# Kernel optimization log

Hardware: AMD Instinct MI355X
Metric: run time of the kernel (lower is better)

## Reference

```python
import jax, jax.numpy as jnp
import numpy as np

C = 256
HEADS = 8
HD = C // HEADS
EPS = 1e-5


def _layernorm(x, g, b):
    mu = jnp.mean(x, axis=-1, keepdims=True)
    var = jnp.var(x, axis=-1, keepdims=True)
    return (x - mu) * jax.lax.rsqrt(var + EPS) * g + b


def setup_inputs() -> dict:
    key = jax.random.key(0)
    ks = jax.random.split(key, 16)
    s = 0.02
    return {
        "x": jax.random.normal(ks[0], (1, C, 64, 64), jnp.float32),
        "bn_gamma": 1.0 + s * jax.random.normal(ks[1], (C,), jnp.float32),
        "bn_beta": s * jax.random.normal(ks[2], (C,), jnp.float32),
        "bn_mean": s * jax.random.normal(ks[3], (C,), jnp.float32),
        "bn_var": jnp.ones((C,), jnp.float32),
        "w_in": s * jax.random.normal(ks[4], (C, C), jnp.float32),
        "b_in": jnp.zeros((C,), jnp.float32),
        "ln1_g": jnp.ones((C,), jnp.float32),
        "ln1_b": jnp.zeros((C,), jnp.float32),
        "w_qkv": s * jax.random.normal(ks[5], (3 * C, C), jnp.float32),
        "b_qkv": jnp.zeros((3 * C,), jnp.float32),
        "w_ap": s * jax.random.normal(ks[6], (C, C), jnp.float32),
        "b_ap": jnp.zeros((C,), jnp.float32),
        "ln2_g": jnp.ones((C,), jnp.float32),
        "ln2_b": jnp.zeros((C,), jnp.float32),
        "w_ff1": s * jax.random.normal(ks[7], (4 * C, C), jnp.float32),
        "b_ff1": jnp.zeros((4 * C,), jnp.float32),
        "w_ff2": s * jax.random.normal(ks[8], (C, 4 * C), jnp.float32),
        "b_ff2": jnp.zeros((C,), jnp.float32),
        "w_out": s * jax.random.normal(ks[9], (C, C), jnp.float32),
        "b_out": jnp.zeros((C,), jnp.float32),
    }


def reference(x, bn_gamma, bn_beta, bn_mean, bn_var, w_in, b_in,
              ln1_g, ln1_b, w_qkv, b_qkv, w_ap, b_ap,
              ln2_g, ln2_b, w_ff1, b_ff1, w_ff2, b_ff2, w_out, b_out):
    b, c, h, w = x.shape
    t = h * w
    x_in = x
    # BatchNorm2d (eval mode: running stats)
    xn = (x - bn_mean[None, :, None, None]) * jax.lax.rsqrt(bn_var + EPS)[None, :, None, None]
    xn = xn * bn_gamma[None, :, None, None] + bn_beta[None, :, None, None]
    # proj_in 1x1 conv -> tokens [b, t, c]
    tok = xn.reshape(b, c, t).transpose(0, 2, 1)
    tok = tok @ w_in.T + b_in
    # transformer block (depth=1)
    y = _layernorm(tok, ln1_g, ln1_b)  # norm1
    qkv = y @ w_qkv.T + b_qkv  # [b, t, 3c], channel split (3, H, hd)
    qkv = qkv.reshape(b, t, 3, HEADS, HD)
    q = qkv[:, :, 0].transpose(0, 2, 1, 3)  # [b, H, t, hd]
    k = qkv[:, :, 1].transpose(0, 2, 1, 3)
    v = qkv[:, :, 2].transpose(0, 2, 1, 3)
    scale = HD ** (-0.5)
    attn = jax.nn.softmax(jnp.einsum('bhqd,bhkd->bhqk', q, k) * scale, axis=-1)
    o = jnp.einsum('bhqk,bhkd->bhqd', attn, v)  # [b, H, t, hd]
    o = o.transpose(0, 2, 1, 3).reshape(b, t, c)  # channels ordered (H, hd)
    o = o @ w_ap.T + b_ap  # attn proj 1x1
    attn_out = o + y  # VanillaAttention residual adds its (normed) input
    tok = tok + attn_out
    # FFN
    z = _layernorm(tok, ln2_g, ln2_b)
    z = jax.nn.gelu(z @ w_ff1.T + b_ff1, approximate=False)
    tok = tok + (z @ w_ff2.T + b_ff2)
    # back to image, proj_out 1x1, outer residual
    x4 = tok.transpose(0, 2, 1).reshape(b, c, h, w)
    out = jnp.einsum('oc,bchw->bohw', w_out, x4) + b_out[None, :, None, None]
    return out + x_in
```

## Files before the change

### kernel.cpp

```cpp
#include <hip/hip_runtime.h>
#include <math.h>

#define T_TOK 4096
#define C_DIM 256
#define EPSF  1e-5f
#define SC_QL (0.17677669529663687f * 1.4426950408889634f)

typedef short  bf16x8  __attribute__((ext_vector_type(8)));
typedef float  f32x4   __attribute__((ext_vector_type(4)));
typedef ushort ushort8 __attribute__((ext_vector_type(8)));

__device__ __forceinline__ short f2bf(float f) {
    unsigned u = __builtin_bit_cast(unsigned, f);
    unsigned r = (u + 0x7FFFu + ((u >> 16) & 1u)) >> 16;
    return (short)r;
}
__device__ __forceinline__ float bf2f(ushort u) {
    return __builtin_bit_cast(float, ((unsigned)u) << 16);
}
__device__ __forceinline__ unsigned pk_bf16(float a, float b) {
    const unsigned ua = __builtin_bit_cast(unsigned, a) + 0x8000u;
    const unsigned ub = __builtin_bit_cast(unsigned, b) + 0x8000u;
    return __builtin_amdgcn_perm(ub, ua, 0x07060302u);
}
#define MFMA16(a, b, c) __builtin_amdgcn_mfma_f32_16x16x32_bf16(a, b, c, 0, 0, 0)

__global__ __launch_bounds__(256) void prep_kernel(
    const float* __restrict__ w_in, const float* __restrict__ w_qkv,
    const float* __restrict__ w_ap, const float* __restrict__ w_ff1,
    const float* __restrict__ w_ff2, const float* __restrict__ w_out,
    const float* __restrict__ b_qkv, const float* __restrict__ b_ff1,
    const float* __restrict__ ln1_g, const float* __restrict__ ln1_b,
    const float* __restrict__ ln2_g, const float* __restrict__ ln2_b,
    ushort* __restrict__ wbuf, float* __restrict__ u_all, float* __restrict__ d_all,
    const float* __restrict__ x, const float* __restrict__ gamma,
    const float* __restrict__ beta, const float* __restrict__ mean,
    const float* __restrict__ var, ushort* __restrict__ tin)
{
    __shared__ float tile[32][33];
    if (blockIdx.x < 896) {
        const int gid = blockIdx.x * 256 + threadIdx.x;
        const int e0 = gid * 4;
        const float* src; int off;
        float4 sc = {1.f, 1.f, 1.f, 1.f};
        if (e0 < 65536)       { src = w_in;  off = e0; }
        else if (e0 < 262144) {
            src = w_qkv; off = e0 - 65536;
            sc = *(const float4*)(ln1_g + (off & 255));
            if (off < 65536) { sc.x *= SC_QL; sc.y *= SC_QL; sc.z *= SC_QL; sc.w *= SC_QL; }
        }
        else if (e0 < 327680) { src = w_ap;  off = e0 - 262144; }
        else if (e0 < 589824) {
            src = w_ff1; off = e0 - 327680;
            sc = *(const float4*)(ln2_g + (off & 255));
        }
        else if (e0 < 851968) { src = w_ff2; off = e0 - 589824; }
        else                  { src = w_out; off = e0 - 851968; }
        const float4 v = *(const float4*)(src + off);
        ushort4 o;
        o.x = (ushort)f2bf(v.x * sc.x); o.y = (ushort)f2bf(v.y * sc.y);
        o.z = (ushort)f2bf(v.z * sc.z); o.w = (ushort)f2bf(v.w * sc.w);
        *(ushort4*)(wbuf + e0) = o;
    } else if (blockIdx.x < 1920) {
        const int bidx = blockIdx.x - 896;
        const int t0 = (bidx & 127) * 32, c0 = (bidx >> 7) * 32;
        const int tx = threadIdx.x & 31, ty = threadIdx.x >> 5;
#pragma unroll
        for (int i = 0; i < 32; i += 8) {
            const int c = c0 + ty + i;
            const float a = rsqrtf(var[c] + EPSF) * gamma[c];
            const float d = beta[c] - mean[c] * a;
            tile[ty + i][tx] = x[c * T_TOK + t0 + tx] * a + d;
        }
        __syncthreads();
#pragma unroll
        for (int i = 0; i < 32; i += 8) {
            const int t = t0 + ty + i;
            tin[t * C_DIM + c0 + tx] = (ushort)f2bf(tile[tx][ty + i]);
        }
    } else {
        const int row = (blockIdx.x - 1920) * 4 + (threadIdx.x >> 6);
        const int lane = threadIdx.x & 63;
        const float* W; const float* gv; const float* bv; float bias; float qs = 1.f;
        if (row < 768) {
            W = w_qkv + (size_t)row * 256; gv = ln1_g; bv = ln1_b; bias = b_qkv[row];
            if (row < 256) qs = SC_QL;
        } else {
            const int r2 = row - 768;
            W = w_ff1 + (size_t)r2 * 256; gv = ln2_g; bv = ln2_b; bias = b_ff1[r2];
        }
        const float4 w4 = *(const float4*)(W + lane * 4);
        const float4 g4 = *(const float4*)(gv + lane * 4);
        const float4 b4 = *(const float4*)(bv + lane * 4);
        float su = w4.x * g4.x + w4.y * g4.y + w4.z * g4.z + w4.w * g4.w;
        float sd = w4.x * b4.x + w4.y * b4.y + w4.z * b4.z + w4.w * b4.w;
#pragma unroll
        for (int off = 32; off > 0; off >>= 1) {
            su += __shfl_xor(su, off);
            sd += __shfl_xor(sd, off);
        }
        if (lane == 0) {
            u_all[row] = qs * su;
            d_all[row] = qs * (sd + bias);
        }
    }
}

__global__ __launch_bounds__(256) void k_lnstats(
    const float* __restrict__ in, float* __restrict__ st)
{
    const int row = blockIdx.x * 4 + (threadIdx.x >> 6);
    const int lane = threadIdx.x & 63;
    const float4 v = *(const float4*)(in + (size_t)row * 256 + lane * 4);
    float s  = v.x + v.y + v.z + v.w;
    float s2 = v.x * v.x + v.y * v.y + v.z * v.z + v.w * v.w;
#pragma unroll
    for (int off = 32; off > 0; off >>= 1) {
        s  += __shfl_xor(s, off);
        s2 += __shfl_xor(s2, off);
    }
    if (lane == 0) {
        const float mu = s * (1.0f / 256.0f);
        const float var = s2 * (1.0f / 256.0f) - mu * mu;
        st[(size_t)row * 2 + 0] = mu;
        st[(size_t)row * 2 + 1] = rsqrtf(var + EPSF);
    }
}


__global__ __launch_bounds__(256) void k_proj_in(
    const ushort* __restrict__ tin, const ushort* __restrict__ wb,
    const float* __restrict__ bias, float* __restrict__ tok0,
    ushort* __restrict__ vbuf)
{
    __shared__ ushort At[16 * 264];
    const int chunk = blockIdx.x & 3, strip = blockIdx.x >> 2;
    const int tid = threadIdx.x, wv = tid >> 6, lane = tid & 63;
    const int c = lane & 15, g = lane >> 4;
    const int col = chunk * 64 + wv * 16 + c;
    const int t0 = strip * 16;

    bf16x8 w[8];
#pragma unroll
    for (int kc = 0; kc < 8; ++kc)
        w[kc] = *(const bf16x8*)(wb + (size_t)col * 256 + kc * 32 + g * 8);
    {
        const int r = tid >> 4, c0 = (tid & 15) * 16;
        *(ushort8*)&At[r * 264 + c0]     = *(const ushort8*)(tin + (size_t)(t0 + r) * 256 + c0);
        *(ushort8*)&At[r * 264 + c0 + 8] = *(const ushort8*)(tin + (size_t)(t0 + r) * 256 + c0 + 8);
    }
    __syncthreads();
    f32x4 acc = {};
#pragma unroll
    for (int kc = 0; kc < 8; ++kc)
        acc = MFMA16(*(const bf16x8*)&At[c * 264 + kc * 32 + g * 8], w[kc], acc);
    const float bb = bias[col];
#pragma unroll
    for (int rr = 0; rr < 4; ++rr) {
        const float v = acc[rr] + bb;
        const size_t idx = (size_t)(t0 + 4 * g + rr) * 256 + col;
        tok0[idx] = v;
        vbuf[idx] = (ushort)f2bf(v);
    }
}

__global__ __launch_bounds__(256) void k_qkv(
    const ushort* __restrict__ vbuf, const ushort* __restrict__ wb,
    const float* __restrict__ lnst, const float* __restrict__ u_all,
    const float* __restrict__ d_all, ushort* __restrict__ qkvb)
{
    __shared__ ushort At[2][16 * 264];
    const int chunk = blockIdx.x % 12, strip = blockIdx.x / 12;
    const int tid = threadIdx.x, wv = tid >> 6, lane = tid & 63;
    const int c = lane & 15, g = lane >> 4;
    const int col = chunk * 64 + wv * 16 + c;
    const int t0 = strip * 32;
    const int r = tid >> 4, c0 = (tid & 15) * 16;

    bf16x8 w[8];
#pragma unroll
    for (int kc = 0; kc < 8; ++kc)
        w[kc] = *(const bf16x8*)(wb + (size_t)col * 256 + kc * 32 + g * 8);
    ushort8 pre0 = *(const ushort8*)(vbuf + (size_t)(t0 + r) * 256 + c0);
    ushort8 pre1 = *(const ushort8*)(vbuf + (size_t)(t0 + r) * 256 + c0 + 8);

    const float u = u_all[col], d = d_all[col];
#pragma unroll
    for (int tile = 0; tile < 2; ++tile) {
        *(ushort8*)&At[tile][r * 264 + c0]     = pre0;
        *(ushort8*)&At[tile][r * 264 + c0 + 8] = pre1;
        __syncthreads();
        if (tile == 0) {
            pre0 = *(const ushort8*)(vbuf + (size_t)(t0 + 16 + r) * 256 + c0);
            pre1 = *(const ushort8*)(vbuf + (size_t)(t0 + 16 + r) * 256 + c0 + 8);
        }
        f32x4 acc = {};
#pragma unroll
        for (int kc = 0; kc < 8; ++kc)
            acc = MFMA16(*(const bf16x8*)&At[tile][c * 264 + kc * 32 + g * 8], w[kc], acc);
        const int tt = t0 + tile * 16;
#pragma unroll
        for (int rr = 0; rr < 4; ++rr) {
            const int row = tt + 4 * g + rr;
            const float mu = lnst[(size_t)row * 2 + 0];
            const float rs = lnst[(size_t)row * 2 + 1];
            qkvb[(size_t)row * 768 + col] = (ushort)f2bf(rs * (acc[rr] - mu * u) + d);
        }
    }
}

__global__ __launch_bounds__(256) void k_attnproj(
    const ushort* __restrict__ opart, const float* __restrict__ lpart,
    const ushort* __restrict__ wb, const float* __restrict__ bias,
    const float* __restrict__ tok0, const float* __restrict__ lnst,
    const float* __restrict__ ln1_g, const float* __restrict__ ln1_b,
    float* __restrict__ tok1, ushort* __restrict__ v2buf)
{
    __shared__ ushort At[16 * 264];
    const int chunk = blockIdx.x & 3, strip = blockIdx.x >> 2;
    const int tid = threadIdx.x, wv = tid >> 6, lane = tid & 63;
    const int c = lane & 15, g = lane >> 4;
    const int col = chunk * 64 + wv * 16 + c;
    const int t0 = strip * 16;

    bf16x8 w[8];
#pragma unroll
    for (int kc = 0; kc < 8; ++kc)
        w[kc] = *(const bf16x8*)(wb + (size_t)col * 256 + kc * 32 + g * 8);
    {
        const int r = tid >> 4, c0 = (tid & 15) * 16;
        const int hh = c0 >> 5;
        const float* lp = lpart + (size_t)(t0 + r) * 32;
        const float inv = 1.0f / (lp[hh] + lp[8 + hh] + lp[16 + hh] + lp[24 + hh]);
        const size_t base = (size_t)(t0 + r) * 256 + c0;
#pragma unroll
        for (int cc = 0; cc < 4; ++cc) {
            const ushort4 a0 = *(const ushort4*)(opart + base + cc * 4);
            const ushort4 a1 = *(const ushort4*)(opart + (1u << 20) + base + cc * 4);
            const ushort4 a2 = *(const ushort4*)(opart + (2u << 20) + base + cc * 4);
            const ushort4 a3 = *(const ushort4*)(opart + (3u << 20) + base + cc * 4);
            unsigned wpk[2];
            wpk[0] = pk_bf16((bf2f(a0.x) + bf2f(a1.x) + bf2f(a2.x) + bf2f(a3.x)) * inv,
                             (bf2f(a0.y) + bf2f(a1.y) + bf2f(a2.y) + bf2f(a3.y)) * inv);
            wpk[1] = pk_bf16((bf2f(a0.z) + bf2f(a1.z) + bf2f(a2.z) + bf2f(a3.z)) * inv,
                             (bf2f(a0.w) + bf2f(a1.w) + bf2f(a2.w) + bf2f(a3.w)) * inv);
            *(ushort4*)&At[r * 264 + c0 + cc * 4] = *(ushort4*)wpk;
        }
    }
    __syncthreads();
    f32x4 acc = {};
#pragma unroll
    for (int kc = 0; kc < 8; ++kc)
        acc = MFMA16(*(const bf16x8*)&At[c * 264 + kc * 32 + g * 8], w[kc], acc);
    const float bb = bias[col];
    const float g1 = ln1_g[col], b1 = ln1_b[col];
#pragma unroll
    for (int rr = 0; rr < 4; ++rr) {
        const int row = t0 + 4 * g + rr;
        const size_t idx = (size_t)row * 256 + col;
        const float t0v = tok0[idx];
        const float mu = lnst[(size_t)row * 2 + 0];
        const float rs = lnst[(size_t)row * 2 + 1];
        const float y = (t0v - mu) * rs * g1 + b1;
        const float v = acc[rr] + bb + y + t0v;
        tok1[idx] = v;
        v2buf[idx] = (ushort)f2bf(v);
    }
}

__global__ __launch_bounds__(256) void k_ff1(
    const ushort* __restrict__ v2buf, const ushort* __restrict__ wb,
    const float* __restrict__ lnst, const float* __restrict__ u_all,
    const float* __restrict__ d_all, ushort* __restrict__ zbuf)
{
    __shared__ ushort At[2][16 * 264];
    const int chunk = blockIdx.x & 15, strip = blockIdx.x >> 4;
    const int tid = threadIdx.x, wv = tid >> 6, lane = tid & 63;
    const int c = lane & 15, g = lane >> 4;
    const int col = chunk * 64 + wv * 16 + c;
    const int t0 = strip * 32;
    const int r = tid >> 4, c0 = (tid & 15) * 16;

    bf16x8 w[8];
#pragma unroll
    for (int kc = 0; kc < 8; ++kc)
        w[kc] = *(const bf16x8*)(wb + (size_t)col * 256 + kc * 32 + g * 8);
    ushort8 pre0 = *(const ushort8*)(v2buf + (size_t)(t0 + r) * 256 + c0);
    ushort8 pre1 = *(const ushort8*)(v2buf + (size_t)(t0 + r) * 256 + c0 + 8);

    const float u = u_all[768 + col], d = d_all[768 + col];
#pragma unroll
    for (int tile = 0; tile < 2; ++tile) {
        *(ushort8*)&At[tile][r * 264 + c0]     = pre0;
        *(ushort8*)&At[tile][r * 264 + c0 + 8] = pre1;
        __syncthreads();
        if (tile == 0) {
            pre0 = *(const ushort8*)(v2buf + (size_t)(t0 + 16 + r) * 256 + c0);
            pre1 = *(const ushort8*)(v2buf + (size_t)(t0 + 16 + r) * 256 + c0 + 8);
        }
        f32x4 acc = {};
#pragma unroll
        for (int kc = 0; kc < 8; ++kc)
            acc = MFMA16(*(const bf16x8*)&At[tile][c * 264 + kc * 32 + g * 8], w[kc], acc);
        const int tt = t0 + tile * 16;
#pragma unroll
        for (int rr = 0; rr < 4; ++rr) {
            const int row = tt + 4 * g + rr;
            const float mu = lnst[(size_t)row * 2 + 0];
            const float rs = lnst[(size_t)row * 2 + 1];
            float v = rs * (acc[rr] - mu * u) + d;
            v = 0.5f * v * (1.0f + erff(v * 0.70710678118654752f));
            zbuf[(size_t)row * 1024 + col] = (ushort)f2bf(v);
        }
    }
}

__global__ __launch_bounds__(256) void k_ff2(
    const ushort* __restrict__ zbuf, const ushort* __restrict__ wb,
    float* __restrict__ pf2)
{
    __shared__ ushort At[2][16 * 520];
    const int chunk = blockIdx.x & 3, half = (blockIdx.x >> 2) & 1, strip = blockIdx.x >> 3;
    const int tid = threadIdx.x, wv = tid >> 6, lane = tid & 63;
    const int c = lane & 15, g = lane >> 4;
    const int col = chunk * 64 + wv * 16 + c;
    const int t0 = strip * 32;
    const int r = tid >> 4, c0 = (tid & 15) * 32;

    bf16x8 w[16];
#pragma unroll
    for (int kc = 0; kc < 16; ++kc)
        w[kc] = *(const bf16x8*)(wb + (size_t)col * 1024 + half * 512 + kc * 32 + g * 8);
    const ushort* zsrc = zbuf + half * 512;
    ushort8 pre[4];
#pragma unroll
    for (int i = 0; i < 4; ++i)
        pre[i] = *(const ushort8*)(zsrc + (size_t)(t0 + r) * 1024 + c0 + i * 8);

#pragma unroll
    for (int tile = 0; tile < 2; ++tile) {
#pragma unroll
        for (int i = 0; i < 4; ++i)
            *(ushort8*)&At[tile][r * 520 + c0 + i * 8] = pre[i];
        __syncthreads();
        if (tile == 0) {
#pragma unroll
            for (int i = 0; i < 4; ++i)
                pre[i] = *(const ushort8*)(zsrc + (size_t)(t0 + 16 + r) * 1024 + c0 + i * 8);
        }
        f32x4 acc = {};
#pragma unroll
        for (int kc = 0; kc < 16; ++kc)
            acc = MFMA16(*(const bf16x8*)&At[tile][c * 520 + kc * 32 + g * 8], w[kc], acc);
        const int tt = t0 + tile * 16;
        float* op = pf2 + (size_t)half * (1u << 20);
#pragma unroll
        for (int rr = 0; rr < 4; ++rr)
            op[(size_t)(tt + 4 * g + rr) * 256 + col] = acc[rr];
    }
}

__global__ __launch_bounds__(256) void k_pout(
    const float* __restrict__ pf2, const float* __restrict__ b_ff2,
    const float* __restrict__ tok1, const ushort* __restrict__ wb,
    const float* __restrict__ b_out, const float* __restrict__ x,
    float* __restrict__ out)
{
    __shared__ ushort At[16 * 264];
    const int chunk = blockIdx.x & 3, strip = blockIdx.x >> 2;
    const int tid = threadIdx.x, wv = tid >> 6, lane = tid & 63;
    const int c = lane & 15, g = lane >> 4;
    const int t0 = strip * 16;

    bf16x8 w[8];
#pragma unroll
    for (int kc = 0; kc < 8; ++kc)
        w[kc] = *(const bf16x8*)(wb +
            (size_t)(chunk * 64 + wv * 16 + c) * 256 + kc * 32 + g * 8);
    {
        const int r = tid >> 4, c0 = (tid & 15) * 16;
        const size_t base = (size_t)(t0 + r) * 256 + c0;
#pragma unroll
        for (int q = 0; q < 4; ++q) {
            const float4 p0 = *(const float4*)(pf2 + base + q * 4);
            const float4 p1 = *(const float4*)(pf2 + (1u << 20) + base + q * 4);
            const float4 tk = *(const float4*)(tok1 + base + q * 4);
            const float4 bf = *(const float4*)(b_ff2 + c0 + q * 4);
            unsigned wpk[2];
            wpk[0] = pk_bf16(p0.x + p1.x + bf.x + tk.x, p0.y + p1.y + bf.y + tk.y);
            wpk[1] = pk_bf16(p0.z + p1.z + bf.z + tk.z, p0.w + p1.w + bf.w + tk.w);
            *(ushort4*)&At[r * 264 + c0 + q * 4] = *(ushort4*)wpk;
        }
    }
    __syncthreads();
    f32x4 acc = {};
#pragma unroll
    for (int kc = 0; kc < 8; ++kc)
        acc = MFMA16(w[kc], *(const bf16x8*)&At[c * 264 + kc * 32 + g * 8], acc);
#pragma unroll
    for (int rr = 0; rr < 4; ++rr) {
        const int och = chunk * 64 + wv * 16 + 4 * g + rr;
        const size_t idx = (size_t)och * T_TOK + t0 + c;
        out[idx] = acc[rr] + b_out[och] + x[idx];
    }
}

#define KS   40
#define VTS  72
#define PS_W 34

__global__ __launch_bounds__(256) void attn_mfma(
    const ushort* __restrict__ qkv, ushort* __restrict__ opart,
    float* __restrict__ lpart)
{
    const int h    = blockIdx.y;
    const int q0   = blockIdx.x << 6;
    const int half = blockIdx.z;
    const int tid  = threadIdx.x;
    const int wv   = tid >> 6, lane = tid & 63;
    const int c    = lane & 15, g = lane >> 4;

    __shared__ ushort Ks[2][64 * KS];
    __shared__ ushort Vt[2][32 * VTS];
    __shared__ float  Ps[4][16 * PS_W];

    const bf16x8 qf = *(const bf16x8*)(qkv + (size_t)(q0 + wv * 16 + c) * 768 + h * 32 + g * 8);

    bf16x8 ones;
#pragma unroll
    for (int i = 0; i < 8; ++i) ones[i] = (short)0x3F80;

    f32x4 oacc0 = {0.f, 0.f, 0.f, 0.f};
    f32x4 oacc1 = {0.f, 0.f, 0.f, 0.f};
    f32x4 oaccl = {0.f, 0.f, 0.f, 0.f};

    const int kr = tid >> 2, kc = (tid & 3) * 8;
    const int vp = tid & 31, vd = (tid >> 5) * 4;
    const ushort* kbase = qkv + 256 + h * 32;
    const ushort* vbase = qkv + 512 + h * 32;

    const int kt0 = half * 16, kt1 = kt0 + 16;
    ushort8 kpre  = *(const ushort8*)(kbase + ((size_t)kt0 * 64 + kr) * 768 + kc);
    ushort4 vpre0 = *(const ushort4*)(vbase + ((size_t)kt0 * 64 + 2 * vp) * 768 + vd);
    ushort4 vpre1 = *(const ushort4*)(vbase + ((size_t)kt0 * 64 + 2 * vp + 1) * 768 + vd);

    int p = 0;
    for (int kt = kt0; kt < kt1; ++kt) {
        *(ushort8*)&Ks[p][kr * KS + kc] = kpre;
        {
            unsigned* vtp = (unsigned*)&Vt[p][0];
            vtp[(vd + 0) * (VTS / 2) + vp] = (unsigned)vpre0.x | ((unsigned)vpre1.x << 16);
            vtp[(vd + 1) * (VTS / 2) + vp] = (unsigned)vpre0.y | ((unsigned)vpre1.y << 16);
            vtp[(vd + 2) * (VTS / 2) + vp] = (unsigned)vpre0.z | ((unsigned)vpre1.z << 16);
            vtp[(vd + 3) * (VTS / 2) + vp] = (unsigned)vpre0.w | ((unsigned)vpre1.w << 16);
        }
        __syncthreads();
        if (kt + 1 < kt1) {
            const size_t t0 = (size_t)(kt + 1) * 64;
            kpre  = *(const ushort8*)(kbase + (t0 + kr) * 768 + kc);
            vpre0 = *(const ushort4*)(vbase + (t0 + 2 * vp) * 768 + vd);
            vpre1 = *(const ushort4*)(vbase + (t0 + 2 * vp + 1) * 768 + vd);
        }

        const ushort* ks = &Ks[p][0];
        const ushort* vt = &Vt[p][0];
        const f32x4 zz = {0.f, 0.f, 0.f, 0.f};
        const bf16x8 k0 = *(const bf16x8*)&ks[(0 * 16 + c) * KS + g * 8];
        const bf16x8 k1 = *(const bf16x8*)&ks[(1 * 16 + c) * KS + g * 8];
        const bf16x8 k2 = *(const bf16x8*)&ks[(2 * 16 + c) * KS + g * 8];
        const bf16x8 k3 = *(const bf16x8*)&ks[(3 * 16 + c) * KS + g * 8];
        const f32x4 s0 = MFMA16(k0, qf, zz);
        const f32x4 s1 = MFMA16(k1, qf, zz);
        const f32x4 s2 = MFMA16(k2, qf, zz);
        const f32x4 s3 = MFMA16(k3, qf, zz);

        float* prow = &Ps[wv][c * PS_W];
        {
            const float e00 = __builtin_amdgcn_exp2f(s0[0]), e01 = __builtin_amdgcn_exp2f(s0[1]);
            const float e02 = __builtin_amdgcn_exp2f(s0[2]), e03 = __builtin_amdgcn_exp2f(s0[3]);
            const float e10 = __builtin_amdgcn_exp2f(s1[0]), e11 = __builtin_amdgcn_exp2f(s1[1]);
            const float e12 = __builtin_amdgcn_exp2f(s1[2]), e13 = __builtin_amdgcn_exp2f(s1[3]);
            const float e20 = __builtin_amdgcn_exp2f(s2[0]), e21 = __builtin_amdgcn_exp2f(s2[1]);
            const float e22 = __builtin_amdgcn_exp2f(s2[2]), e23 = __builtin_amdgcn_exp2f(s2[3]);
            const float e30 = __builtin_amdgcn_exp2f(s3[0]), e31 = __builtin_amdgcn_exp2f(s3[1]);
            const float e32 = __builtin_amdgcn_exp2f(s3[2]), e33 = __builtin_amdgcn_exp2f(s3[3]);
            prow[0 * 8 + 2 * g + 0] = __builtin_bit_cast(float, pk_bf16(e00, e01));
            prow[0 * 8 + 2 * g + 1] = __builtin_bit_cast(float, pk_bf16(e02, e03));
            prow[1 * 8 + 2 * g + 0] = __builtin_bit_cast(float, pk_bf16(e10, e11));
            prow[1 * 8 + 2 * g + 1] = __builtin_bit_cast(float, pk_bf16(e12, e13));
            prow[2 * 8 + 2 * g + 0] = __builtin_bit_cast(float, pk_bf16(e20, e21));
            prow[2 * 8 + 2 * g + 1] = __builtin_bit_cast(float, pk_bf16(e22, e23));
            prow[3 * 8 + 2 * g + 0] = __builtin_bit_cast(float, pk_bf16(e30, e31));
            prow[3 * 8 + 2 * g + 1] = __builtin_bit_cast(float, pk_bf16(e32, e33));
        }
#pragma unroll
        for (int ch = 0; ch < 2; ++ch) {
            const float2 pA = *(const float2*)&prow[ch * 16 + 4 * g];
            const float2 pB = *(const float2*)&prow[ch * 16 + 4 * g + 2];
            unsigned pw[4];
            pw[0] = __builtin_bit_cast(unsigned, pA.x);
            pw[1] = __builtin_bit_cast(unsigned, pA.y);
            pw[2] = __builtin_bit_cast(unsigned, pB.x);
            pw[3] = __builtin_bit_cast(unsigned, pB.y);
            const bf16x8 pf = *(const bf16x8*)pw;
            const bf16x8 v0 = *(const bf16x8*)&vt[(c)      * VTS + ch * 32 + g * 8];
            const bf16x8 v1 = *(const bf16x8*)&vt[(16 + c) * VTS + ch * 32 + g * 8];
            oacc0 = MFMA16(pf, v0, oacc0);
            oacc1 = MFMA16(pf, v1, oacc1);
            oaccl = MFMA16(pf, ones, oaccl);
        }
        p ^= 1;
        __syncthreads();
    }

    {
        ushort* op = opart + (size_t)half * (1u << 20) + (size_t)(q0 + wv * 16) * 256 + h * 32;
#pragma unroll
        for (int rr = 0; rr < 4; ++rr) {
            op[(4 * g + rr) * 256 + c]      = (ushort)f2bf(oacc0[rr]);
            op[(4 * g + rr) * 256 + 16 + c] = (ushort)f2bf(oacc1[rr]);
        }
        if (c == 0) {
#pragma unroll
            for (int rr = 0; rr < 4; ++rr)
                lpart[(size_t)(q0 + wv * 16 + 4 * g + rr) * 32 + half * 8 + h] = oaccl[rr];
        }
    }
}

extern "C" void kernel_launch(void* const* d_in, const int* in_sizes, int n_in,
                              void* d_out, int out_size, void* d_ws, size_t ws_size,
                              hipStream_t stream)
{
    const float* x     = (const float*)d_in[0];
    const float* bn_g  = (const float*)d_in[1];
    const float* bn_b  = (const float*)d_in[2];
    const float* bn_m  = (const float*)d_in[3];
    const float* bn_v  = (const float*)d_in[4];
    const float* w_in  = (const float*)d_in[5];
    const float* b_in  = (const float*)d_in[6];
    const float* ln1_g = (const float*)d_in[7];
    const float* ln1_b = (const float*)d_in[8];
    const float* w_qkv = (const float*)d_in[9];
    const float* b_qkv = (const float*)d_in[10];
    const float* w_ap  = (const float*)d_in[11];
    const float* b_ap  = (const float*)d_in[12];
    const float* ln2_g = (const float*)d_in[13];
    const float* ln2_b = (const float*)d_in[14];
    const float* w_ff1 = (const float*)d_in[15];
    const float* b_ff1 = (const float*)d_in[16];
    const float* w_ff2 = (const float*)d_in[17];
    const float* b_ff2 = (const float*)d_in[18];
    const float* w_out = (const float*)d_in[19];
    const float* b_out = (const float*)d_in[20];
    float* out = (float*)d_out;
    float* ws  = (float*)d_ws;

    const size_t MF = 1u << 20;
    float*  tok0   = ws;
    float*  tok1   = ws + MF;
    float*  lnst1  = ws + 2 * MF;
    float*  lnst2  = ws + 2 * MF + 8192;
    ushort* vbuf   = (ushort*)(ws + 2 * MF + MF / 2);
    ushort* qkv_bf = (ushort*)(ws + 3 * MF);
    ushort* tin_bf = (ushort*)(ws + 4 * MF + MF / 2);
    ushort* opart  = tin_bf;
    ushort* v2buf  = (ushort*)(ws + 6 * MF + MF / 2);
    ushort* zbuf   = (ushort*)(ws + 7 * MF);
    float*  lpart  = ws + 9 * MF;
    float*  pf2    = ws + 9 * MF + MF / 4;
    ushort* wbuf   = (ushort*)(ws + 11 * MF + MF / 2);
    const ushort* wb_in  = wbuf;
    const ushort* wb_qkv = wbuf + 65536;
    const ushort* wb_ap  = wbuf + 262144;
    const ushort* wb_ff1 = wbuf + 327680;
    const ushort* wb_ff2 = wbuf + 589824;
    const ushort* wb_out = wbuf + 851968;
    float* u_all = (float*)(wbuf + 917504);
    float* d_all = u_all + 1792;

    prep_kernel<<<2368, 256, 0, stream>>>(
        w_in, w_qkv, w_ap, w_ff1, w_ff2, w_out,
        b_qkv, b_ff1, ln1_g, ln1_b, ln2_g, ln2_b,
        wbuf, u_all, d_all,
        x, bn_g, bn_b, bn_m, bn_v, tin_bf);
    k_proj_in<<<1024, 256, 0, stream>>>(tin_bf, wb_in, b_in, tok0, vbuf);
    k_lnstats<<<1024, 256, 0, stream>>>(tok0, lnst1);
    k_qkv<<<1536, 256, 0, stream>>>(vbuf, wb_qkv, lnst1, u_all, d_all, qkv_bf);
    attn_mfma<<<dim3(64, 8, 4), 256, 0, stream>>>(qkv_bf, opart, lpart);
    k_attnproj<<<1024, 256, 0, stream>>>(opart, lpart, wb_ap, b_ap, tok0, lnst1,
                                         ln1_g, ln1_b, tok1, v2buf);
    k_lnstats<<<1024, 256, 0, stream>>>(tok1, lnst2);
    k_ff1<<<2048, 256, 0, stream>>>(v2buf, wb_ff1, lnst2, u_all, d_all, zbuf);
    k_ff2<<<1024, 256, 0, stream>>>(zbuf, wb_ff2, pf2);
    k_pout<<<1024, 256, 0, stream>>>(pf2, b_ff2, tok1, wb_out, b_out, x, out);
}
```

Before: 210.6 us.

## Write V transposed from QKV kernel and load it directly in attention

The QKV projection now writes the V third of its output in a channel-major transposed buffer, so the attention kernel can fill its V tile in shared memory with one 16-byte load and store per thread. This replaces the per-element interleaved transpose stores it used before. The P-row padding changes from 34 to 33 floats, which turns the paired float2 reads into scalar reads. The attention launch is split into two launches of half the key range each. The cost is an extra workspace buffer and an additional kernel launch.

Result: slower. 217.5 us (+3.3%).

```diff
diff --git a/kernel.cpp b/kernel.cpp
--- a/kernel.cpp
+++ b/kernel.cpp
@@ -167,7 +167,8 @@
 __global__ __launch_bounds__(256) void k_qkv(
     const ushort* __restrict__ vbuf, const ushort* __restrict__ wb,
     const float* __restrict__ lnst, const float* __restrict__ u_all,
-    const float* __restrict__ d_all, ushort* __restrict__ qkvb)
+    const float* __restrict__ d_all, ushort* __restrict__ qkvb,
+    ushort* __restrict__ vT)
 {
     __shared__ ushort At[2][16 * 264];
     const int chunk = blockIdx.x % 12, strip = blockIdx.x / 12;
@@ -199,12 +200,25 @@
         for (int kc = 0; kc < 8; ++kc)
             acc = MFMA16(*(const bf16x8*)&At[tile][c * 264 + kc * 32 + g * 8], w[kc], acc);
         const int tt = t0 + tile * 16;
-#pragma unroll
-        for (int rr = 0; rr < 4; ++rr) {
-            const int row = tt + 4 * g + rr;
-            const float mu = lnst[(size_t)row * 2 + 0];
-            const float rs = lnst[(size_t)row * 2 + 1];
-            qkvb[(size_t)row * 768 + col] = (ushort)f2bf(rs * (acc[rr] - mu * u) + d);
+        if (col < 512) {
+#pragma unroll
+            for (int rr = 0; rr < 4; ++rr) {
+                const int row = tt + 4 * g + rr;
+                const float mu = lnst[(size_t)row * 2 + 0];
+                const float rs = lnst[(size_t)row * 2 + 1];
+                qkvb[(size_t)row * 768 + col] = (ushort)f2bf(rs * (acc[rr] - mu * u) + d);
+            }
+        } else {
+            ushort4 ov;
+            ushort* o = (ushort*)&ov;
+#pragma unroll
+            for (int rr = 0; rr < 4; ++rr) {
+                const int row = tt + 4 * g + rr;
+                const float mu = lnst[(size_t)row * 2 + 0];
+                const float rs = lnst[(size_t)row * 2 + 1];
+                o[rr] = (ushort)f2bf(rs * (acc[rr] - mu * u) + d);
+            }
+            *(ushort4*)(vT + (size_t)(col - 512) * 4096 + tt + 4 * g) = ov;
         }
     }
 }
@@ -407,15 +421,15 @@
 
 #define KS   40
 #define VTS  72
-#define PS_W 34
+#define PS_W 33
 
 __global__ __launch_bounds__(256) void attn_mfma(
-    const ushort* __restrict__ qkv, ushort* __restrict__ opart,
-    float* __restrict__ lpart)
+    const ushort* __restrict__ qkv, const ushort* __restrict__ vT,
+    ushort* __restrict__ opart, float* __restrict__ lpart, int zb)
 {
     const int h    = blockIdx.y;
     const int q0   = blockIdx.x << 6;
-    const int half = blockIdx.z;
+    const int half = zb + blockIdx.z;
     const int tid  = threadIdx.x;
     const int wv   = tid >> 6, lane = tid & 63;
     const int c    = lane & 15, g = lane >> 4;
@@ -435,31 +449,22 @@
     f32x4 oaccl = {0.f, 0.f, 0.f, 0.f};
 
     const int kr = tid >> 2, kc = (tid & 3) * 8;
-    const int vp = tid & 31, vd = (tid >> 5) * 4;
+    const int vd3 = tid >> 3, kc8 = (tid & 7) * 8;
     const ushort* kbase = qkv + 256 + h * 32;
-    const ushort* vbase = qkv + 512 + h * 32;
+    const ushort* vtb   = vT + (size_t)h * 32 * 4096;
 
     const int kt0 = half * 16, kt1 = kt0 + 16;
-    ushort8 kpre  = *(const ushort8*)(kbase + ((size_t)kt0 * 64 + kr) * 768 + kc);
-    ushort4 vpre0 = *(const ushort4*)(vbase + ((size_t)kt0 * 64 + 2 * vp) * 768 + vd);
-    ushort4 vpre1 = *(const ushort4*)(vbase + ((size_t)kt0 * 64 + 2 * vp + 1) * 768 + vd);
+    ushort8 kpre = *(const ushort8*)(kbase + ((size_t)kt0 * 64 + kr) * 768 + kc);
+    ushort8 vpre = *(const ushort8*)(vtb + (size_t)vd3 * 4096 + kt0 * 64 + kc8);
 
     int p = 0;
     for (int kt = kt0; kt < kt1; ++kt) {
         *(ushort8*)&Ks[p][kr * KS + kc] = kpre;
-        {
-            unsigned* vtp = (unsigned*)&Vt[p][0];
-            vtp[(vd + 0) * (VTS / 2) + vp] = (unsigned)vpre0.x | ((unsigned)vpre1.x << 16);
-            vtp[(vd + 1) * (VTS / 2) + vp] = (unsigned)vpre0.y | ((unsigned)vpre1.y << 16);
-            vtp[(vd + 2) * (VTS / 2) + vp] = (unsigned)vpre0.z | ((unsigned)vpre1.z << 16);
-            vtp[(vd + 3) * (VTS / 2) + vp] = (unsigned)vpre0.w | ((unsigned)vpre1.w << 16);
-        }
+        *(ushort8*)&Vt[p][vd3 * VTS + kc8] = vpre;
         __syncthreads();
         if (kt + 1 < kt1) {
-            const size_t t0 = (size_t)(kt + 1) * 64;
-            kpre  = *(const ushort8*)(kbase + (t0 + kr) * 768 + kc);
-            vpre0 = *(const ushort4*)(vbase + (t0 + 2 * vp) * 768 + vd);
-            vpre1 = *(const ushort4*)(vbase + (t0 + 2 * vp + 1) * 768 + vd);
+            kpre = *(const ushort8*)(kbase + ((size_t)(kt + 1) * 64 + kr) * 768 + kc);
+            vpre = *(const ushort8*)(vtb + (size_t)vd3 * 4096 + (kt + 1) * 64 + kc8);
         }
 
         const ushort* ks = &Ks[p][0];
@@ -495,13 +500,11 @@
         }
 #pragma unroll
         for (int ch = 0; ch < 2; ++ch) {
-            const float2 pA = *(const float2*)&prow[ch * 16 + 4 * g];
-            const float2 pB = *(const float2*)&prow[ch * 16 + 4 * g + 2];
             unsigned pw[4];
-            pw[0] = __builtin_bit_cast(unsigned, pA.x);
-            pw[1] = __builtin_bit_cast(unsigned, pA.y);
-            pw[2] = __builtin_bit_cast(unsigned, pB.x);
-            pw[3] = __builtin_bit_cast(unsigned, pB.y);
+            pw[0] = __builtin_bit_cast(unsigned, prow[ch * 16 + 4 * g + 0]);
+            pw[1] = __builtin_bit_cast(unsigned, prow[ch * 16 + 4 * g + 1]);
+            pw[2] = __builtin_bit_cast(unsigned, prow[ch * 16 + 4 * g + 2]);
+            pw[3] = __builtin_bit_cast(unsigned, prow[ch * 16 + 4 * g + 3]);
             const bf16x8 pf = *(const bf16x8*)pw;
             const bf16x8 v0 = *(const bf16x8*)&vt[(c)      * VTS + ch * 32 + g * 8];
             const bf16x8 v1 = *(const bf16x8*)&vt[(16 + c) * VTS + ch * 32 + g * 8];
@@ -570,6 +573,7 @@
     float*  lpart  = ws + 9 * MF;
     float*  pf2    = ws + 9 * MF + MF / 4;
     ushort* wbuf   = (ushort*)(ws + 11 * MF + MF / 2);
+    ushort* vT     = (ushort*)(ws + 12 * MF);
     const ushort* wb_in  = wbuf;
     const ushort* wb_qkv = wbuf + 65536;
     const ushort* wb_ap  = wbuf + 262144;
@@ -586,8 +590,9 @@
         x, bn_g, bn_b, bn_m, bn_v, tin_bf);
     k_proj_in<<<1024, 256, 0, stream>>>(tin_bf, wb_in, b_in, tok0, vbuf);
     k_lnstats<<<1024, 256, 0, stream>>>(tok0, lnst1);
-    k_qkv<<<1536, 256, 0, stream>>>(vbuf, wb_qkv, lnst1, u_all, d_all, qkv_bf);
-    attn_mfma<<<dim3(64, 8, 4), 256, 0, stream>>>(qkv_bf, opart, lpart);
+    k_qkv<<<1536, 256, 0, stream>>>(vbuf, wb_qkv, lnst1, u_all, d_all, qkv_bf, vT);
+    attn_mfma<<<dim3(64, 8, 2), 256, 0, stream>>>(qkv_bf, vT, opart, lpart, 0);
+    attn_mfma<<<dim3(64, 8, 2), 256, 0, stream>>>(qkv_bf, vT, opart, lpart, 2);
     k_attnproj<<<1024, 256, 0, stream>>>(opart, lpart, wb_ap, b_ap, tok0, lnst1,
                                          ln1_g, ln1_b, tok1, v2buf);
     k_lnstats<<<1024, 256, 0, stream>>>(tok1, lnst2);
```
